# Optimization experiments

Hardware: AMD Instinct MI355X
Metric: run time of the kernel (lower is better)

The kernel has to match this reference:

```python
import jax, jax.numpy as jnp
import numpy as np

ALPHA = 0.2   # LeakyReLU negative slope (init arg alpha)
H = 256       # hidden_dim
U = 1024      # user pairs -> 2U user nodes
M = 64        # UAV nodes
D = 2 * U     # uniform out-degree per UAV (edges sorted by source)
N = 2 * U + M
E = M * D


def _lstm_dir(x, w_ih, w_hh, b):
    # x: [T, B, I] -> outputs [T, B, Hc]; b = b_ih + b_hh (they only ever add)
    Hc = w_hh.shape[1]
    B = x.shape[1]
    def step(carry, xt):
        h, c = carry
        g = xt @ w_ih.T + h @ w_hh.T + b          # [B, 4*Hc], gate order i,f,g,o
        i, f, gg, o = jnp.split(g, 4, axis=-1)
        c = jax.nn.sigmoid(f) * c + jax.nn.sigmoid(i) * jnp.tanh(gg)
        h = jax.nn.sigmoid(o) * jnp.tanh(c)
        return (h, c), h
    h0 = jnp.zeros((B, Hc), x.dtype)
    _, hs = jax.lax.scan(step, (h0, h0), x)
    return hs


def _bilstm(x, wih, whh, b):
    # wih: [2, 4Hc, I]; whh: [2, 4Hc, Hc]; b: [2, 4Hc]; dir 0 = fwd, 1 = reverse
    fwd = _lstm_dir(x, wih[0], whh[0], b[0])
    rev = _lstm_dir(x[::-1], wih[1], whh[1], b[1])[::-1]
    return jnp.concatenate([fwd, rev], axis=-1)   # [T, B, 2*Hc]


def _mlp2(h, w1, b1, w2, b2):
    h = jax.nn.relu(h @ w1.T + b1)
    return jax.nn.relu(h @ w2.T + b2)


def _forward(x, edge_index, users_num,
             ul_wih, ul_whh, ul_b, uav_lin_w, uav_lin_b,
             msg_w1, msg_b1, msg_w2, msg_b2,
             wq_w, wq_b, wr_w, wr_b, att_w, att_b,
             upd_w1, upd_b1, upd_w2, upd_b2,
             uavl_wih, uavl_whh, uavl_b, lin2_w, lin2_b):
    Un = users_num
    n = x.shape[0]
    m = n - 2 * Un
    # ---- users bidirectional LSTM over the pair (seq_len=2, batch=U) ----
    seq = jnp.stack([x[:Un], x[Un:2 * Un]], axis=0)        # [2, U, 2]
    users = _bilstm(seq, ul_wih, ul_whh, ul_b)             # [2, U, H]
    users = jnp.concatenate([users[0], users[1]], axis=0)  # [2U, H]
    uavs = x[2 * Un:] @ uav_lin_w.T + uav_lin_b            # [M, H]
    h = jnp.concatenate([users, uavs], axis=0)             # [N, H]
    # ---- message passing (flow target_to_source: i=src, aggregate at src) ----
    src, tgt = edge_index[0], edge_index[1]
    xi = h[src]                                            # [E, H]
    xj = h[tgt]                                            # [E, H]
    msg = _mlp2(jnp.concatenate([xi, xj], axis=1), msg_w1, msg_b1, msg_w2, msg_b2)  # [E, H]
    q = xi @ wq_w.T + wq_b
    r = msg @ wr_w.T + wr_b
    a = jax.nn.leaky_relu(jnp.concatenate([q, r], axis=1) @ att_w.T + att_b, ALPHA)  # [E,1]
    # segment softmax: edges sorted by source, uniform degree -> reshape [M, D]
    a = jax.nn.softmax(a.reshape(m, -1), axis=1).reshape(-1, 1)
    # ---- scatter-mean aggregate over source index ----
    agg = jax.ops.segment_sum(a * msg, src, num_segments=n)          # [N, H]
    cnt = jax.ops.segment_sum(jnp.ones((src.shape[0],), x.dtype), src, num_segments=n)
    agg = agg / jnp.maximum(cnt, 1.0)[:, None]
    # ---- update ----
    h2 = _mlp2(jnp.concatenate([agg, h], axis=1), upd_w1, upd_b1, upd_w2, upd_b2)  # [N, H]
    uav_seq = h2[2 * Un:][:, None, :]                      # [M, 1, H]
    uav_out = _bilstm(uav_seq, uavl_wih, uavl_whh, uavl_b)[:, 0, :]  # [M, H]
    out = jnp.concatenate([h2[:2 * Un], uav_out], axis=0)
    return jax.nn.sigmoid(out @ lin2_w.T + lin2_b)         # [N, 2]


def setup_inputs():
    key = jax.random.key(0)
    ks = iter(jax.random.split(key, 32))
    p = lambda *s: jax.random.normal(next(ks), s, jnp.float32) * 0.05
    Hc = H // 2
    x = jax.random.uniform(next(ks), (N, 2), jnp.float32)
    src = jnp.repeat(2 * U + jnp.arange(M), D)
    tgt = jnp.tile(jnp.arange(2 * U), M)
    edge_index = jnp.stack([src, tgt]).astype(jnp.int32)
    return dict(
        x=x, edge_index=edge_index, users_num=U,
        ul_wih=p(2, 4 * Hc, 2), ul_whh=p(2, 4 * Hc, Hc), ul_b=p(2, 4 * Hc),
        uav_lin_w=p(H, 2), uav_lin_b=p(H),
        msg_w1=p(H, 2 * H), msg_b1=p(H), msg_w2=p(H, H), msg_b2=p(H),
        wq_w=p(H, H), wq_b=p(H), wr_w=p(H, H), wr_b=p(H),
        att_w=p(1, 2 * H), att_b=p(1),
        upd_w1=p(H, 2 * H), upd_b1=p(H), upd_w2=p(H, H), upd_b2=p(H),
        uavl_wih=p(2, 4 * Hc, H), uavl_whh=p(2, 4 * Hc, Hc), uavl_b=p(2, 4 * Hc),
        lin2_w=p(2, H), lin2_b=p(2),
    )


def reference(x, edge_index, users_num,
              ul_wih, ul_whh, ul_b, uav_lin_w, uav_lin_b,
              msg_w1, msg_b1, msg_w2, msg_b2,
              wq_w, wq_b, wr_w, wr_b, att_w, att_b,
              upd_w1, upd_b1, upd_w2, upd_b2,
              uavl_wih, uavl_whh, uavl_b, lin2_w, lin2_b):
    return _forward(x, edge_index, users_num,
                    ul_wih, ul_whh, ul_b, uav_lin_w, uav_lin_b,
                    msg_w1, msg_b1, msg_w2, msg_b2,
                    wq_w, wq_b, wr_w, wr_b, att_w, att_b,
                    upd_w1, upd_b1, upd_w2, upd_b2,
                    uavl_wih, uavl_whh, uavl_b, lin2_w, lin2_b)
```

## Files before the change

### kernel.cpp

```cpp
#include <hip/hip_runtime.h>
#include <hip/hip_bf16.h>
#include <math.h>

#define UQ   1024
#define NUQ  2048
#define MQ   64
#define NN   2112
#define HD   256

typedef __attribute__((ext_vector_type(4))) float f32x4;
typedef __attribute__((ext_vector_type(8))) __bf16 bf16x8;

#define OFF_HB    0u
#define OFF_HUF   65536u
#define OFF_PUBF  1146880u
#define OFF_PB    2195456u
#define OFF_SPR   2260992u
#define OFF_ATT   2261248u
#define OFF_WHHT  2263552u
#define OFF_WIHT  2787840u
#define OFF_W1F   3836416u
#define OFF_W2F   4098560u
#define OFF_UW1F  4229632u
#define OFF_UW2F  4491776u
#define OFF_CREC  4622848u
#define OFF_H2U   5155328u

__device__ __forceinline__ float sigm(float v) { return 1.f / (1.f + expf(-v)); }

__device__ __forceinline__ int huf_idx(int row, int k) {
  return (((row >> 6) * 8 + (k >> 5)) * 4 + ((row >> 4) & 3)) * 512 +
         (((k >> 3) & 3) * 16 + (row & 15)) * 8 + (k & 7);
}
__device__ __forceinline__ int pubf_idx(int row, int k) {
  return (((row >> 8) * 8 + (k >> 5)) * 16 + ((row >> 4) & 15)) * 512 +
         (((k >> 3) & 3) * 16 + (row & 15)) * 8 + (k & 7);
}

__device__ __forceinline__ void gl16(const void* g, void* l) {
  __builtin_amdgcn_global_load_lds((const __attribute__((address_space(1))) void*)g,
                                   (__attribute__((address_space(3))) void*)l, 16, 0, 0);
}

__device__ void tile_transpose_perm(const float* __restrict__ in, int in_ld,
                                    float* __restrict__ out, int out_ld,
                                    int k0, int c0) {
  __shared__ float ldt[64][68];
  const int t = threadIdx.x;
  {
    const int ci = t >> 2, kq = t & 3;
    const int c = c0 + ci;
    const int row = (c & 3) * 128 + (c >> 2);
    const float* src = in + row * in_ld + k0 + kq * 16;
#pragma unroll
    for (int e = 0; e < 4; ++e)
      *(f32x4*)&ldt[ci][kq * 16 + e * 4] = *(const f32x4*)(src + e * 4);
  }
  __syncthreads();
  {
    const int kk = t >> 2, cq = t & 3;
    float* dst = out + (k0 + kk) * out_ld + c0 + cq * 16;
#pragma unroll
    for (int e4 = 0; e4 < 4; ++e4) {
      f32x4 v;
#pragma unroll
      for (int j = 0; j < 4; ++j) v[j] = ldt[cq * 16 + e4 * 4 + j][kk];
      *(f32x4*)(dst + e4 * 4) = v;
    }
  }
}

template<int K>
__device__ void frag_cast16(const float* __restrict__ W, int j0, __bf16* __restrict__ frag) {
  __shared__ float ldc[16][K + 4];
  const int t = threadIdx.x;
  {
    const int jr = t >> 4, kq = t & 15;
    const float* src = W + (j0 + jr) * K + kq * (K / 16);
#pragma unroll
    for (int e = 0; e < K / 64; ++e)
      *(f32x4*)&ldc[jr][kq * (K / 16) + e * 4] = *(const f32x4*)(src + e * 4);
  }
  __syncthreads();
  const int f = j0 >> 4;
  constexpr int nks = K >> 5;
  constexpr int thr_per_ks = 256 / nks;
  constexpr int q_per_thr = 512 / thr_per_ks;
  const int ks = t / thr_per_ks;
  const int q0 = (t % thr_per_ks) * q_per_thr;
#pragma unroll
  for (int h = 0; h < q_per_thr / 8; ++h) {
    bf16x8 v;
#pragma unroll
    for (int e = 0; e < 8; ++e) {
      int q = q0 + h * 8 + e;
      int lane = q >> 3;
      v[e] = (__bf16)ldc[lane & 15][ks * 32 + (lane >> 4) * 8 + (q & 7)];
    }
    *(bf16x8*)(frag + (ks * 16 + f) * 512 + q0 + h * 8) = v;
  }
}

__global__ __launch_bounds__(256) void k0_prep(
    const float* __restrict__ ul_whh, const float* __restrict__ uavl_wih,
    const float* __restrict__ msg_w1, const float* __restrict__ msg_w2,
    const float* __restrict__ upd_w1, const float* __restrict__ upd_w2,
    const float* __restrict__ att_w,  const float* __restrict__ att_b,
    const float* __restrict__ wq_w,   const float* __restrict__ wq_b,
    const float* __restrict__ wr_w,   const float* __restrict__ wr_b,
    char* __restrict__ ws)
{
  const int b = blockIdx.x, t = threadIdx.x;
  if (b < 32) {
    const int dir = b >> 4, tile = b & 15;
    tile_transpose_perm(ul_whh + dir * 65536, 128,
                        (float*)(ws + OFF_WHHT) + dir * 65536, 512,
                        (tile >> 3) * 64, (tile & 7) * 64);
  } else if (b < 96) {
    const int b2 = b - 32, dir = b2 >> 5, tile = b2 & 31;
    tile_transpose_perm(uavl_wih + dir * 131072, 256,
                        (float*)(ws + OFF_WIHT) + dir * 131072, 512,
                        (tile >> 3) * 64, (tile & 7) * 64);
  } else if (b < 112) {
    frag_cast16<256>(msg_w2, (b - 96) * 16, (__bf16*)(ws + OFF_W2F));
  } else if (b < 128) {
    frag_cast16<512>(msg_w1, (b - 112) * 16, (__bf16*)(ws + OFF_W1F));
  } else if (b < 144) {
    frag_cast16<512>(upd_w1, (b - 128) * 16, (__bf16*)(ws + OFF_UW1F));
  } else if (b < 160) {
    frag_cast16<256>(upd_w2, (b - 144) * 16, (__bf16*)(ws + OFF_UW2F));
  } else {
    float* wqa = (float*)(ws + OFF_ATT);
    float* vv  = wqa + 256;
    float* c0  = wqa + 512;
    float sa = 0.f, sr = 0.f;
    for (int j = 0; j < 256; ++j) {
      sa += att_w[j]       * wq_w[j * 256 + t];
      sr += att_w[256 + j] * wr_w[j * 256 + t];
    }
    wqa[t] = sa; vv[t] = sr;
    __shared__ float red[256];
    red[t] = att_w[t] * wq_b[t] + att_w[256 + t] * wr_b[t];
    __syncthreads();
    for (int s = 128; s > 0; s >>= 1) { if (t < s) red[t] += red[t + s]; __syncthreads(); }
    if (t == 0) c0[0] = red[0] + att_b[0];
  }
}

__global__ __launch_bounds__(256) void k1_embed(
    const float* __restrict__ x, const float* __restrict__ ul_wih,
    const float* __restrict__ ul_b, const float* __restrict__ uav_lin_w,
    const float* __restrict__ uav_lin_b, char* __restrict__ ws)
{
  __bf16* huf = (__bf16*)(ws + OFF_HUF);
  const int b = blockIdx.x, tid = threadIdx.x;
  if (b < 256) {
    const float* whhT = (const float*)(ws + OFF_WHHT);
    const int dir = tid >> 7, hc = tid & 127;
    const int u0 = b * 4;
    float wx[4], wy[4], bb[4];
#pragma unroll
    for (int g = 0; g < 4; ++g) {
      int row = g * 128 + hc;
      wx[g] = ul_wih[dir * 1024 + row * 2 + 0];
      wy[g] = ul_wih[dir * 1024 + row * 2 + 1];
      bb[g] = ul_b[dir * 512 + row];
    }
    __shared__ float h1s[2][128][4];
    __shared__ float hout[8][260];
    float c1[4], h1v[4], in1x[4], in1y[4];
#pragma unroll
    for (int uu = 0; uu < 4; ++uu) {
      int u = u0 + uu;
      float ax = x[u * 2], ay = x[u * 2 + 1];
      float bx = x[(UQ + u) * 2], by = x[(UQ + u) * 2 + 1];
      float i0x = dir ? bx : ax, i0y = dir ? by : ay;
      in1x[uu] = dir ? ax : bx; in1y[uu] = dir ? ay : by;
      float gv[4];
#pragma unroll
      for (int g = 0; g < 4; ++g) gv[g] = wx[g] * i0x + wy[g] * i0y + bb[g];
      float ii = sigm(gv[0]), gg = tanhf(gv[2]), oo = sigm(gv[3]);
      c1[uu] = ii * gg;
      h1v[uu] = oo * tanhf(c1[uu]);
      h1s[dir][hc][uu] = h1v[uu];
    }
    __syncthreads();
    float acc[4][4];
#pragma unroll
    for (int uu = 0; uu < 4; ++uu)
#pragma unroll
      for (int g = 0; g < 4; ++g) acc[uu][g] = wx[g] * in1x[uu] + wy[g] * in1y[uu] + bb[g];
    for (int k = 0; k < 128; ++k) {
      f32x4 hv  = *(const f32x4*)&h1s[dir][k][0];
      f32x4 wv4 = *(const f32x4*)(whhT + dir * 65536 + k * 512 + hc * 4);
#pragma unroll
      for (int uu = 0; uu < 4; ++uu)
#pragma unroll
        for (int g = 0; g < 4; ++g) acc[uu][g] += hv[uu] * wv4[g];
    }
    const int col = dir * 128 + hc;
#pragma unroll
    for (int uu = 0; uu < 4; ++uu) {
      float ii = sigm(acc[uu][0]), ff = sigm(acc[uu][1]);
      float gg = tanhf(acc[uu][2]), oo = sigm(acc[uu][3]);
      float c2 = ff * c1[uu] + ii * gg;
      float h2v = oo * tanhf(c2);
      float va = dir ? h2v : h1v[uu];
      float vb = dir ? h1v[uu] : h2v;
      hout[uu][col] = va;
      hout[4 + uu][col] = vb;
    }
    __syncthreads();
    {
      const int lr = tid >> 5, c = tid & 31;
      bf16x8 v;
#pragma unroll
      for (int e = 0; e < 8; ++e) v[e] = (__bf16)hout[lr][c * 8 + e];
      const int node = (lr < 4) ? (u0 + lr) : (UQ + u0 + lr - 4);
      *(bf16x8*)(huf + huf_idx(node, c * 8)) = v;
    }
  } else {
    float* hb = (float*)(ws + OFF_HB);
    const int j = tid;
    const int mb = (b - 256) * 16;
    for (int m = mb; m < mb + 16; ++m) {
      float xa = x[(NUQ + m) * 2], xb = x[(NUQ + m) * 2 + 1];
      float val = xa * uav_lin_w[j * 2] + xb * uav_lin_w[j * 2 + 1] + uav_lin_b[j];
      hb[m * 256 + j] = val;
      huf[huf_idx(NUQ + m, j)] = (__bf16)val;
    }
  }
}

template<int NKS>
__device__ __forceinline__ void frag_gemm_acc(const __bf16* __restrict__ Abase,
                                              const __bf16* __restrict__ Bbase,
                                              f32x4 acc[4][4]) {
  const int lane = threadIdx.x & 63;
  const int cg = threadIdx.x >> 6;
  for (int ks = 0; ks < NKS; ++ks) {
    bf16x8 Af[4], Bf[4];
#pragma unroll
    for (int g = 0; g < 4; ++g)
      Af[g] = *(const bf16x8*)(Abase + ((ks * 4 + g) * 64 + lane) * 8);
#pragma unroll
    for (int f = 0; f < 4; ++f)
      Bf[f] = *(const bf16x8*)(Bbase + ((ks * 16 + cg * 4 + f) * 64 + lane) * 8);
#pragma unroll
    for (int g = 0; g < 4; ++g)
#pragma unroll
      for (int f = 0; f < 4; ++f)
        acc[g][f] = __builtin_amdgcn_mfma_f32_16x16x32_bf16(Af[g], Bf[f], acc[g][f], 0, 0, 0);
  }
}

__global__ __launch_bounds__(256) void k2_proj(const float* __restrict__ msg_b1,
                                               char* __restrict__ ws)
{
  const __bf16* huf = (const __bf16*)(ws + OFF_HUF);
  const __bf16* w1f = (const __bf16*)(ws + OFF_W1F);
  const int b = blockIdx.x;
  const int lane = threadIdx.x & 63, cg = threadIdx.x >> 6;
  const int cl = lane & 15, g16 = lane >> 4;
  if (b < 32) {
    f32x4 acc[4][4] = {};
    frag_gemm_acc<8>(huf + b * 16384, w1f + 65536, acc);
    __bf16* pubf = (__bf16*)(ws + OFF_PUBF);
#pragma unroll
    for (int g = 0; g < 4; ++g)
#pragma unroll
      for (int f = 0; f < 4; ++f)
#pragma unroll
        for (int r = 0; r < 4; ++r) {
          int row = b * 64 + g * 16 + g16 * 4 + r;
          int col = cg * 64 + f * 16 + cl;
          pubf[pubf_idx(row, col)] = (__bf16)acc[g][f][r];
        }
  } else if (b == 32) {
    f32x4 acc[4][4] = {};
    frag_gemm_acc<8>(huf + 32 * 16384, w1f, acc);
    float* pb = (float*)(ws + OFF_PB);
#pragma unroll
    for (int g = 0; g < 4; ++g)
#pragma unroll
      for (int f = 0; f < 4; ++f)
#pragma unroll
        for (int r = 0; r < 4; ++r) {
          int row = g * 16 + g16 * 4 + r;
          int col = cg * 64 + f * 16 + cl;
          pb[row * 256 + col] = acc[g][f][r] + msg_b1[col];
        }
  } else {
    const float* hb  = (const float*)(ws + OFF_HB);
    const float* wqa = (const float*)(ws + OFF_ATT);
    const float* c0  = wqa + 512;
    float* spr = (float*)(ws + OFF_SPR);
    const int t = threadIdx.x;
    if (t < 64) {
      float s = 0.f;
      for (int k = 0; k < 256; ++k) s += hb[t * 256 + k] * wqa[k];
      spr[t] = s + c0[0];
    }
  }
}

__global__ __launch_bounds__(1024, 2) void k3_edge(const float* __restrict__ msg_b2,
                                                   char* __restrict__ ws)
{
  const char*  PUBF = (const char*)(ws + OFF_PUBF);
  const float* PB   = (const float*)(ws + OFF_PB);
  const float* spr  = (const float*)(ws + OFF_SPR);
  const float* vv   = (const float*)(ws + OFF_ATT) + 256;
  const char*  W2F  = (const char*)(ws + OFF_W2F);
  float* crec = (float*)(ws + OFF_CREC);

  __shared__ __align__(16) char bufA[2][16384];
  __shared__ __align__(16) char bufB[2][16384];
  __shared__ float plds[16][64];
  __shared__ float redmax[16], wds[16];
  __shared__ float wvs[4][256];

  const int m = blockIdx.x >> 3, ch = blockIdx.x & 7;
  const int tid = threadIdx.x, wave = tid >> 6, lane = tid & 63;
  const int cl = lane & 15, g16 = lane >> 4;
  const int rg = wave >> 2, cg = wave & 3;
  const float sm = spr[m];
  const char* Asrc = PUBF + ch * 131072;
  const float* pbm = PB + m * 256;

  {
    bf16x8 araw = *(const bf16x8*)(Asrc + wave * 1024 + lane * 16);
    gl16(W2F + wave * 1024 + lane * 16, &bufB[0][wave * 1024]);
    const float* pbp = pbm + (lane >> 4) * 8;
    f32x4 p0 = *(const f32x4*)pbp, p1 = *(const f32x4*)(pbp + 4);
    bf16x8 a;
#pragma unroll
    for (int r = 0; r < 4; ++r) {
      a[r]     = (__bf16)fmaxf((float)araw[r]     + p0[r], 0.f);
      a[4 + r] = (__bf16)fmaxf((float)araw[4 + r] + p1[r], 0.f);
    }
    *(bf16x8*)(&bufA[0][wave * 1024 + lane * 16]) = a;
  }
  __syncthreads();

  f32x4 acc[4][4] = {};
  for (int ks = 0; ks < 8; ++ks) {
    const int cur = ks & 1;
    bf16x8 arn{};
    f32x4 pn0{}, pn1{};
    if (ks < 7) {
      arn = *(const bf16x8*)(Asrc + (ks + 1) * 16384 + wave * 1024 + lane * 16);
      gl16(W2F + (ks + 1) * 16384 + wave * 1024 + lane * 16, &bufB[cur ^ 1][wave * 1024]);
      const float* pbp = pbm + (ks + 1) * 32 + (lane >> 4) * 8;
      pn0 = *(const f32x4*)pbp;
      pn1 = *(const f32x4*)(pbp + 4);
    }
    bf16x8 Af[4], Bf[4];
#pragma unroll
    for (int g = 0; g < 4; ++g)
      Af[g] = *(const bf16x8*)(&bufA[cur][((rg * 4 + g) * 64 + lane) * 16]);
#pragma unroll
    for (int f = 0; f < 4; ++f)
      Bf[f] = *(const bf16x8*)(&bufB[cur][((cg * 4 + f) * 64 + lane) * 16]);
#pragma unroll
    for (int g = 0; g < 4; ++g)
#pragma unroll
      for (int f = 0; f < 4; ++f)
        acc[g][f] = __builtin_amdgcn_mfma_f32_16x16x32_bf16(Af[g], Bf[f], acc[g][f], 0, 0, 0);
    if (ks < 7) {
      bf16x8 a;
#pragma unroll
      for (int r = 0; r < 4; ++r) {
        a[r]     = (__bf16)fmaxf((float)arn[r]     + pn0[r], 0.f);
        a[4 + r] = (__bf16)fmaxf((float)arn[4 + r] + pn1[r], 0.f);
      }
      *(bf16x8*)(&bufA[cur ^ 1][wave * 1024 + lane * 16]) = a;
    }
    __syncthreads();
  }

  float p[4][4] = {};
#pragma unroll
  for (int f = 0; f < 4; ++f) {
    const int j = cg * 64 + f * 16 + cl;
    const float b2j = msg_b2[j], vj = vv[j];
#pragma unroll
    for (int g = 0; g < 4; ++g)
#pragma unroll
      for (int r = 0; r < 4; ++r) {
        float mv = fmaxf(acc[g][f][r] + b2j, 0.f);
        acc[g][f][r] = mv;
        p[g][r] += mv * vj;
      }
  }
#pragma unroll
  for (int mask = 1; mask < 16; mask <<= 1)
#pragma unroll
    for (int g = 0; g < 4; ++g)
#pragma unroll
      for (int r = 0; r < 4; ++r) p[g][r] += __shfl_xor(p[g][r], mask);
  if (cl == 0) {
#pragma unroll
    for (int g = 0; g < 4; ++g)
#pragma unroll
      for (int r = 0; r < 4; ++r) plds[wave][g * 16 + g16 * 4 + r] = p[g][r];
  }
  __syncthreads();

  float lr[4][4], wm = -3.4e38f;
#pragma unroll
  for (int g = 0; g < 4; ++g)
#pragma unroll
    for (int r = 0; r < 4; ++r) {
      int row = g * 16 + g16 * 4 + r;
      float l = plds[rg * 4 + 0][row] + plds[rg * 4 + 1][row] +
                plds[rg * 4 + 2][row] + plds[rg * 4 + 3][row] + sm;
      l = l > 0.f ? l : 0.2f * l;
      lr[g][r] = l;
      wm = fmaxf(wm, l);
    }
  wm = fmaxf(wm, __shfl_xor(wm, 16));
  wm = fmaxf(wm, __shfl_xor(wm, 32));
  if (lane == 0) redmax[wave] = wm;
  __syncthreads();
  float Mc = redmax[0];
#pragma unroll
  for (int i = 1; i < 16; ++i) Mc = fmaxf(Mc, redmax[i]);

  float e[4][4], ds = 0.f;
#pragma unroll
  for (int g = 0; g < 4; ++g)
#pragma unroll
    for (int r = 0; r < 4; ++r) { e[g][r] = __expf(lr[g][r] - Mc); ds += e[g][r]; }
  ds += __shfl_xor(ds, 16);
  ds += __shfl_xor(ds, 32);
  if (lane == 0) wds[wave] = ds;

#pragma unroll
  for (int f = 0; f < 4; ++f) {
    float w = 0.f;
#pragma unroll
    for (int g = 0; g < 4; ++g)
#pragma unroll
      for (int r = 0; r < 4; ++r) w += e[g][r] * acc[g][f][r];
    w += __shfl_xor(w, 16);
    w += __shfl_xor(w, 32);
    if (g16 == 0) wvs[rg][cg * 64 + f * 16 + cl] = w;
  }
  __syncthreads();

  float* rec = crec + (m * 8 + ch) * 260;
  if (tid < 256) rec[tid] = wvs[0][tid] + wvs[1][tid] + wvs[2][tid] + wvs[3][tid];
  if (tid == 0) rec[256] = Mc;
  if (tid == 1) rec[257] = wds[0] + wds[4] + wds[8] + wds[12];
}

__global__ __launch_bounds__(256) void k56_update(
    const float* __restrict__ upd_b1, const float* __restrict__ upd_b2,
    const float* __restrict__ lin2_w, const float* __restrict__ lin2_b,
    float* __restrict__ out, char* __restrict__ ws)
{
  const __bf16* huf  = (const __bf16*)(ws + OFF_HUF);
  const __bf16* uw1f = (const __bf16*)(ws + OFF_UW1F);
  const __bf16* uw2f = (const __bf16*)(ws + OFF_UW2F);

  __shared__ __align__(16) __bf16 l1f[8 * 4 * 512];
  __shared__ __align__(16) __bf16 aggf[8 * 4 * 512];
  __shared__ float scs[64][8];
  __shared__ float sS[64];
  __shared__ float l2p[4][64][2];

  const int b = blockIdx.x, tid = threadIdx.x;
  const int lane = tid & 63, cg = tid >> 6;
  const int cl = lane & 15, g16 = lane >> 4;

  f32x4 acc[4][4] = {};
  if (b < 32) {
    frag_gemm_acc<8>(huf + b * 16384, uw1f + 8 * 16 * 512, acc);
  } else {
    const float* crec = (const float*)(ws + OFF_CREC);
    if (tid < 64) {
      const int m = tid;
      float mx = -3.4e38f;
      for (int c = 0; c < 8; ++c) mx = fmaxf(mx, crec[(m * 8 + c) * 260 + 256]);
      float S = 0.f;
      for (int c = 0; c < 8; ++c) {
        float sc = __expf(crec[(m * 8 + c) * 260 + 256] - mx);
        scs[m][c] = sc;
        S += sc * crec[(m * 8 + c) * 260 + 257];
      }
      sS[m] = S;
    }
    __syncthreads();
    for (int m = 0; m < 64; ++m) {
      float A = 0.f;
#pragma unroll
      for (int c = 0; c < 8; ++c) A += scs[m][c] * crec[(m * 8 + c) * 260 + tid];
      float agg = A / sS[m] * (1.f / 2048.f);
      aggf[((tid >> 5) * 4 + (m >> 4)) * 512 + (((tid >> 3) & 3) * 16 + (m & 15)) * 8 + (tid & 7)] =
          (__bf16)agg;
    }
    __syncthreads();
    const __bf16* hufu = huf + 32 * 16384;
    for (int ks = 0; ks < 8; ++ks) {
      bf16x8 Af[4], Bf[4];
#pragma unroll
      for (int g = 0; g < 4; ++g)
        Af[g] = *(const bf16x8*)(aggf + ((ks * 4 + g) * 64 + lane) * 8);
#pragma unroll
      for (int f = 0; f < 4; ++f)
        Bf[f] = *(const bf16x8*)(uw1f + ((ks * 16 + cg * 4 + f) * 64 + lane) * 8);
#pragma unroll
      for (int g = 0; g < 4; ++g)
#pragma unroll
        for (int f = 0; f < 4; ++f)
          acc[g][f] = __builtin_amdgcn_mfma_f32_16x16x32_bf16(Af[g], Bf[f], acc[g][f], 0, 0, 0);
    }
    for (int ks = 8; ks < 16; ++ks) {
      bf16x8 Af[4], Bf[4];
#pragma unroll
      for (int g = 0; g < 4; ++g)
        Af[g] = *(const bf16x8*)(hufu + (((ks - 8) * 4 + g) * 64 + lane) * 8);
#pragma unroll
      for (int f = 0; f < 4; ++f)
        Bf[f] = *(const bf16x8*)(uw1f + ((ks * 16 + cg * 4 + f) * 64 + lane) * 8);
#pragma unroll
      for (int g = 0; g < 4; ++g)
#pragma unroll
        for (int f = 0; f < 4; ++f)
          acc[g][f] = __builtin_amdgcn_mfma_f32_16x16x32_bf16(Af[g], Bf[f], acc[g][f], 0, 0, 0);
    }
  }

#pragma unroll
  for (int g = 0; g < 4; ++g)
#pragma unroll
    for (int f = 0; f < 4; ++f) {
      const int col = cg * 64 + f * 16 + cl;
      const float b1 = upd_b1[col];
#pragma unroll
      for (int r = 0; r < 4; ++r) {
        const int rl = g * 16 + g16 * 4 + r;
        float v = fmaxf(acc[g][f][r] + b1, 0.f);
        l1f[((col >> 5) * 4 + g) * 512 + (((col >> 3) & 3) * 16 + (rl & 15)) * 8 + (col & 7)] =
            (__bf16)v;
      }
    }
  __syncthreads();

  f32x4 a2[4][4] = {};
  for (int ks = 0; ks < 8; ++ks) {
    bf16x8 Af[4], Bf[4];
#pragma unroll
    for (int g = 0; g < 4; ++g)
      Af[g] = *(const bf16x8*)(l1f + ((ks * 4 + g) * 64 + lane) * 8);
#pragma unroll
    for (int f = 0; f < 4; ++f)
      Bf[f] = *(const bf16x8*)(uw2f + ((ks * 16 + cg * 4 + f) * 64 + lane) * 8);
#pragma unroll
    for (int g = 0; g < 4; ++g)
#pragma unroll
      for (int f = 0; f < 4; ++f)
        a2[g][f] = __builtin_amdgcn_mfma_f32_16x16x32_bf16(Af[g], Bf[f], a2[g][f], 0, 0, 0);
  }

  if (b < 32) {
    float d0[4][4] = {}, d1[4][4] = {};
#pragma unroll
    for (int f = 0; f < 4; ++f) {
      const int col = cg * 64 + f * 16 + cl;
      const float b2 = upd_b2[col];
      const float w0 = lin2_w[col], w1 = lin2_w[256 + col];
#pragma unroll
      for (int g = 0; g < 4; ++g)
#pragma unroll
        for (int r = 0; r < 4; ++r) {
          float hv = fmaxf(a2[g][f][r] + b2, 0.f);
          d0[g][r] += hv * w0;
          d1[g][r] += hv * w1;
        }
    }
#pragma unroll
    for (int mask = 1; mask < 16; mask <<= 1)
#pragma unroll
      for (int g = 0; g < 4; ++g)
#pragma unroll
        for (int r = 0; r < 4; ++r) {
          d0[g][r] += __shfl_xor(d0[g][r], mask);
          d1[g][r] += __shfl_xor(d1[g][r], mask);
        }
    if (cl == 0) {
#pragma unroll
      for (int g = 0; g < 4; ++g)
#pragma unroll
        for (int r = 0; r < 4; ++r) {
          l2p[cg][g * 16 + g16 * 4 + r][0] = d0[g][r];
          l2p[cg][g * 16 + g16 * 4 + r][1] = d1[g][r];
        }
    }
    __syncthreads();
    if (tid < 64) {
      float s0 = l2p[0][tid][0] + l2p[1][tid][0] + l2p[2][tid][0] + l2p[3][tid][0] + lin2_b[0];
      float s1 = l2p[0][tid][1] + l2p[1][tid][1] + l2p[2][tid][1] + l2p[3][tid][1] + lin2_b[1];
      const int row = b * 64 + tid;
      out[row * 2 + 0] = 1.f / (1.f + expf(-s0));
      out[row * 2 + 1] = 1.f / (1.f + expf(-s1));
    }
  } else {
    float* h2u = (float*)(ws + OFF_H2U);
#pragma unroll
    for (int g = 0; g < 4; ++g)
#pragma unroll
      for (int f = 0; f < 4; ++f) {
        const int col = cg * 64 + f * 16 + cl;
        const float b2 = upd_b2[col];
#pragma unroll
        for (int r = 0; r < 4; ++r) {
          const int rl = g * 16 + g16 * 4 + r;
          h2u[rl * 256 + col] = fmaxf(a2[g][f][r] + b2, 0.f);
        }
      }
  }
}

__global__ __launch_bounds__(256) void k7_final(
    const float* __restrict__ uavl_b, const float* __restrict__ lin2_w,
    const float* __restrict__ lin2_b, float* __restrict__ out, char* __restrict__ ws)
{
  const float* h2u = (const float*)(ws + OFF_H2U);
  const int b = blockIdx.x, tid = threadIdx.x;
  const float* wihT = (const float*)(ws + OFF_WIHT);
  __shared__ float xs[256], uo[256];
  xs[tid] = h2u[b * 256 + tid];
  __syncthreads();
  const int dir = tid >> 7, hc = tid & 127;
  float a4[4] = {0.f, 0.f, 0.f, 0.f};
  for (int k = 0; k < 256; ++k) {
    float xv = xs[k];
    f32x4 wv4 = *(const f32x4*)(wihT + dir * 131072 + k * 512 + hc * 4);
#pragma unroll
    for (int g = 0; g < 4; ++g) a4[g] += xv * wv4[g];
  }
  float bb[4];
#pragma unroll
  for (int g = 0; g < 4; ++g) bb[g] = uavl_b[dir * 512 + g * 128 + hc];
  float ii = sigm(a4[0] + bb[0]);
  float gg = tanhf(a4[2] + bb[2]);
  float oo = sigm(a4[3] + bb[3]);
  float cc = ii * gg;
  uo[dir * 128 + hc] = oo * tanhf(cc);
  __syncthreads();
  float p0 = uo[tid] * lin2_w[tid];
  float p1 = uo[tid] * lin2_w[256 + tid];
#pragma unroll
  for (int mask = 1; mask < 64; mask <<= 1) {
    p0 += __shfl_xor(p0, mask);
    p1 += __shfl_xor(p1, mask);
  }
  __shared__ float r0s[4], r1s[4];
  const int lane = tid & 63, wv = tid >> 6;
  if (lane == 0) { r0s[wv] = p0; r1s[wv] = p1; }
  __syncthreads();
  if (tid == 0) {
    float d0 = r0s[0] + r0s[1] + r0s[2] + r0s[3] + lin2_b[0];
    float d1 = r1s[0] + r1s[1] + r1s[2] + r1s[3] + lin2_b[1];
    out[(NUQ + b) * 2 + 0] = 1.f / (1.f + expf(-d0));
    out[(NUQ + b) * 2 + 1] = 1.f / (1.f + expf(-d1));
  }
}

extern "C" void kernel_launch(void* const* d_in, const int* in_sizes, int n_in,
                              void* d_out, int out_size, void* d_ws, size_t ws_size,
                              hipStream_t stream)
{
  const float* x         = (const float*)d_in[0];
  const float* ul_wih    = (const float*)d_in[3];
  const float* ul_whh    = (const float*)d_in[4];
  const float* ul_b      = (const float*)d_in[5];
  const float* uav_lin_w = (const float*)d_in[6];
  const float* uav_lin_b = (const float*)d_in[7];
  const float* msg_w1    = (const float*)d_in[8];
  const float* msg_b1    = (const float*)d_in[9];
  const float* msg_w2    = (const float*)d_in[10];
  const float* msg_b2    = (const float*)d_in[11];
  const float* wq_w      = (const float*)d_in[12];
  const float* wq_b      = (const float*)d_in[13];
  const float* wr_w      = (const float*)d_in[14];
  const float* wr_b      = (const float*)d_in[15];
  const float* att_w     = (const float*)d_in[16];
  const float* att_b     = (const float*)d_in[17];
  const float* upd_w1    = (const float*)d_in[18];
  const float* upd_b1    = (const float*)d_in[19];
  const float* upd_w2    = (const float*)d_in[20];
  const float* upd_b2    = (const float*)d_in[21];
  const float* uavl_wih  = (const float*)d_in[22];
  const float* uavl_b    = (const float*)d_in[24];
  const float* lin2_w    = (const float*)d_in[25];
  const float* lin2_b    = (const float*)d_in[26];
  char* ws = (char*)d_ws;
  float* out = (float*)d_out;

  k0_prep<<<dim3(161), dim3(256), 0, stream>>>(ul_whh, uavl_wih, msg_w1, msg_w2, upd_w1,
                                               upd_w2, att_w, att_b, wq_w, wq_b, wr_w, wr_b, ws);
  k1_embed<<<dim3(260), dim3(256), 0, stream>>>(x, ul_wih, ul_b, uav_lin_w, uav_lin_b, ws);
  k2_proj<<<dim3(34), dim3(256), 0, stream>>>(msg_b1, ws);
  k3_edge<<<dim3(512), dim3(1024), 0, stream>>>(msg_b2, ws);
  k56_update<<<dim3(33), dim3(256), 0, stream>>>(upd_b1, upd_b2, lin2_w, lin2_b, out, ws);
  k7_final<<<dim3(64), dim3(256), 0, stream>>>(uavl_b, lin2_w, lin2_b, out, ws);
}
```

Baseline: 110.8 us.

## Split GEMM kernels into finer row blocks and split final gate GEMV over K

After: 94.51 us. 14.7% less time.

```diff
diff --git a/kernel.cpp b/kernel.cpp
--- a/kernel.cpp
+++ b/kernel.cpp
@@ -25,6 +25,7 @@
 #define OFF_UW2F  4491776u
 #define OFF_CREC  4622848u
 #define OFF_H2U   5155328u
+#define OFF_PART  5220864u
 
 __device__ __forceinline__ float sigm(float v) { return 1.f / (1.f + expf(-v)); }
 
@@ -232,22 +233,22 @@
   }
 }
 
-template<int NKS>
-__device__ __forceinline__ void frag_gemm_acc(const __bf16* __restrict__ Abase,
-                                              const __bf16* __restrict__ Bbase,
-                                              f32x4 acc[4][4]) {
+template<int G, int NKS>
+__device__ __forceinline__ void frag_gemm_acc_g(const __bf16* __restrict__ Abase, int g0,
+                                                const __bf16* __restrict__ Bbase,
+                                                f32x4 acc[G][4]) {
   const int lane = threadIdx.x & 63;
   const int cg = threadIdx.x >> 6;
   for (int ks = 0; ks < NKS; ++ks) {
-    bf16x8 Af[4], Bf[4];
-#pragma unroll
-    for (int g = 0; g < 4; ++g)
-      Af[g] = *(const bf16x8*)(Abase + ((ks * 4 + g) * 64 + lane) * 8);
+    bf16x8 Af[G], Bf[4];
+#pragma unroll
+    for (int g = 0; g < G; ++g)
+      Af[g] = *(const bf16x8*)(Abase + ((ks * 4 + g0 + g) * 64 + lane) * 8);
 #pragma unroll
     for (int f = 0; f < 4; ++f)
       Bf[f] = *(const bf16x8*)(Bbase + ((ks * 16 + cg * 4 + f) * 64 + lane) * 8);
 #pragma unroll
-    for (int g = 0; g < 4; ++g)
+    for (int g = 0; g < G; ++g)
 #pragma unroll
       for (int f = 0; f < 4; ++f)
         acc[g][f] = __builtin_amdgcn_mfma_f32_16x16x32_bf16(Af[g], Bf[f], acc[g][f], 0, 0, 0);
@@ -262,23 +263,23 @@
   const int b = blockIdx.x;
   const int lane = threadIdx.x & 63, cg = threadIdx.x >> 6;
   const int cl = lane & 15, g16 = lane >> 4;
-  if (b < 32) {
-    f32x4 acc[4][4] = {};
-    frag_gemm_acc<8>(huf + b * 16384, w1f + 65536, acc);
+  if (b < 64) {
+    f32x4 acc[2][4] = {};
+    frag_gemm_acc_g<2, 8>(huf + (b >> 1) * 16384, (b & 1) * 2, w1f + 65536, acc);
     __bf16* pubf = (__bf16*)(ws + OFF_PUBF);
 #pragma unroll
-    for (int g = 0; g < 4; ++g)
+    for (int g = 0; g < 2; ++g)
 #pragma unroll
       for (int f = 0; f < 4; ++f)
 #pragma unroll
         for (int r = 0; r < 4; ++r) {
-          int row = b * 64 + g * 16 + g16 * 4 + r;
+          int row = b * 32 + g * 16 + g16 * 4 + r;
           int col = cg * 64 + f * 16 + cl;
           pubf[pubf_idx(row, col)] = (__bf16)acc[g][f][r];
         }
-  } else if (b == 32) {
+  } else if (b == 64) {
     f32x4 acc[4][4] = {};
-    frag_gemm_acc<8>(huf + 32 * 16384, w1f, acc);
+    frag_gemm_acc_g<4, 8>(huf + 32 * 16384, 0, w1f, acc);
     float* pb = (float*)(ws + OFF_PB);
 #pragma unroll
     for (int g = 0; g < 4; ++g)
@@ -324,14 +325,15 @@
   const int tid = threadIdx.x, wave = tid >> 6, lane = tid & 63;
   const int cl = lane & 15, g16 = lane >> 4;
   const int rg = wave >> 2, cg = wave & 3;
+  const int rot = (m + ch) & 7;
   const float sm = spr[m];
   const char* Asrc = PUBF + ch * 131072;
   const float* pbm = PB + m * 256;
 
   {
-    bf16x8 araw = *(const bf16x8*)(Asrc + wave * 1024 + lane * 16);
-    gl16(W2F + wave * 1024 + lane * 16, &bufB[0][wave * 1024]);
-    const float* pbp = pbm + (lane >> 4) * 8;
+    bf16x8 araw = *(const bf16x8*)(Asrc + rot * 16384 + wave * 1024 + lane * 16);
+    gl16(W2F + rot * 16384 + wave * 1024 + lane * 16, &bufB[0][wave * 1024]);
+    const float* pbp = pbm + rot * 32 + (lane >> 4) * 8;
     f32x4 p0 = *(const f32x4*)pbp, p1 = *(const f32x4*)(pbp + 4);
     bf16x8 a;
 #pragma unroll
@@ -344,14 +346,15 @@
   __syncthreads();
 
   f32x4 acc[4][4] = {};
-  for (int ks = 0; ks < 8; ++ks) {
-    const int cur = ks & 1;
+  for (int i = 0; i < 8; ++i) {
+    const int cur = i & 1;
     bf16x8 arn{};
     f32x4 pn0{}, pn1{};
-    if (ks < 7) {
-      arn = *(const bf16x8*)(Asrc + (ks + 1) * 16384 + wave * 1024 + lane * 16);
-      gl16(W2F + (ks + 1) * 16384 + wave * 1024 + lane * 16, &bufB[cur ^ 1][wave * 1024]);
-      const float* pbp = pbm + (ks + 1) * 32 + (lane >> 4) * 8;
+    if (i < 7) {
+      const int ksn = (i + 1 + rot) & 7;
+      arn = *(const bf16x8*)(Asrc + ksn * 16384 + wave * 1024 + lane * 16);
+      gl16(W2F + ksn * 16384 + wave * 1024 + lane * 16, &bufB[cur ^ 1][wave * 1024]);
+      const float* pbp = pbm + ksn * 32 + (lane >> 4) * 8;
       pn0 = *(const f32x4*)pbp;
       pn1 = *(const f32x4*)(pbp + 4);
     }
@@ -362,12 +365,14 @@
 #pragma unroll
     for (int f = 0; f < 4; ++f)
       Bf[f] = *(const bf16x8*)(&bufB[cur][((cg * 4 + f) * 64 + lane) * 16]);
+    __builtin_amdgcn_s_setprio(1);
 #pragma unroll
     for (int g = 0; g < 4; ++g)
 #pragma unroll
       for (int f = 0; f < 4; ++f)
         acc[g][f] = __builtin_amdgcn_mfma_f32_16x16x32_bf16(Af[g], Bf[f], acc[g][f], 0, 0, 0);
-    if (ks < 7) {
+    __builtin_amdgcn_s_setprio(0);
+    if (i < 7) {
       bf16x8 a;
 #pragma unroll
       for (int r = 0; r < 4; ++r) {
@@ -464,68 +469,70 @@
   const __bf16* uw1f = (const __bf16*)(ws + OFF_UW1F);
   const __bf16* uw2f = (const __bf16*)(ws + OFF_UW2F);
 
-  __shared__ __align__(16) __bf16 l1f[8 * 4 * 512];
-  __shared__ __align__(16) __bf16 aggf[8 * 4 * 512];
-  __shared__ float scs[64][8];
-  __shared__ float sS[64];
-  __shared__ float l2p[4][64][2];
+  __shared__ __align__(16) __bf16 l1f[8 * 2 * 512];
+  __shared__ __align__(16) __bf16 aggf[8 * 2 * 512];
+  __shared__ float scs[32][8];
+  __shared__ float sS[32];
+  __shared__ float l2p[4][32][2];
 
   const int b = blockIdx.x, tid = threadIdx.x;
   const int lane = tid & 63, cg = tid >> 6;
   const int cl = lane & 15, g16 = lane >> 4;
 
-  f32x4 acc[4][4] = {};
-  if (b < 32) {
-    frag_gemm_acc<8>(huf + b * 16384, uw1f + 8 * 16 * 512, acc);
+  f32x4 acc[2][4] = {};
+  if (b < 64) {
+    frag_gemm_acc_g<2, 8>(huf + (b >> 1) * 16384, (b & 1) * 2, uw1f + 8 * 16 * 512, acc);
   } else {
+    const int m0 = (b - 64) * 32;
     const float* crec = (const float*)(ws + OFF_CREC);
-    if (tid < 64) {
-      const int m = tid;
+    if (tid < 32) {
+      const int m = m0 + tid;
       float mx = -3.4e38f;
       for (int c = 0; c < 8; ++c) mx = fmaxf(mx, crec[(m * 8 + c) * 260 + 256]);
       float S = 0.f;
       for (int c = 0; c < 8; ++c) {
         float sc = __expf(crec[(m * 8 + c) * 260 + 256] - mx);
-        scs[m][c] = sc;
+        scs[tid][c] = sc;
         S += sc * crec[(m * 8 + c) * 260 + 257];
       }
-      sS[m] = S;
+      sS[tid] = S;
     }
     __syncthreads();
-    for (int m = 0; m < 64; ++m) {
+    for (int ml = 0; ml < 32; ++ml) {
       float A = 0.f;
 #pragma unroll
-      for (int c = 0; c < 8; ++c) A += scs[m][c] * crec[(m * 8 + c) * 260 + tid];
-      float agg = A / sS[m] * (1.f / 2048.f);
-      aggf[((tid >> 5) * 4 + (m >> 4)) * 512 + (((tid >> 3) & 3) * 16 + (m & 15)) * 8 + (tid & 7)] =
+      for (int c = 0; c < 8; ++c) A += scs[ml][c] * crec[((m0 + ml) * 8 + c) * 260 + tid];
+      float agg = A / sS[ml] * (1.f / 2048.f);
+      aggf[((tid >> 5) * 2 + (ml >> 4)) * 512 + (((tid >> 3) & 3) * 16 + (ml & 15)) * 8 + (tid & 7)] =
           (__bf16)agg;
     }
     __syncthreads();
+    const int g0 = (b - 64) * 2;
     const __bf16* hufu = huf + 32 * 16384;
     for (int ks = 0; ks < 8; ++ks) {
-      bf16x8 Af[4], Bf[4];
-#pragma unroll
-      for (int g = 0; g < 4; ++g)
-        Af[g] = *(const bf16x8*)(aggf + ((ks * 4 + g) * 64 + lane) * 8);
+      bf16x8 Af[2], Bf[4];
+#pragma unroll
+      for (int g = 0; g < 2; ++g)
+        Af[g] = *(const bf16x8*)(aggf + ((ks * 2 + g) * 64 + lane) * 8);
 #pragma unroll
       for (int f = 0; f < 4; ++f)
         Bf[f] = *(const bf16x8*)(uw1f + ((ks * 16 + cg * 4 + f) * 64 + lane) * 8);
 #pragma unroll
-      for (int g = 0; g < 4; ++g)
+      for (int g = 0; g < 2; ++g)
 #pragma unroll
         for (int f = 0; f < 4; ++f)
           acc[g][f] = __builtin_amdgcn_mfma_f32_16x16x32_bf16(Af[g], Bf[f], acc[g][f], 0, 0, 0);
     }
     for (int ks = 8; ks < 16; ++ks) {
-      bf16x8 Af[4], Bf[4];
-#pragma unroll
-      for (int g = 0; g < 4; ++g)
-        Af[g] = *(const bf16x8*)(hufu + (((ks - 8) * 4 + g) * 64 + lane) * 8);
+      bf16x8 Af[2], Bf[4];
+#pragma unroll
+      for (int g = 0; g < 2; ++g)
+        Af[g] = *(const bf16x8*)(hufu + (((ks - 8) * 4 + g0 + g) * 64 + lane) * 8);
 #pragma unroll
       for (int f = 0; f < 4; ++f)
         Bf[f] = *(const bf16x8*)(uw1f + ((ks * 16 + cg * 4 + f) * 64 + lane) * 8);
 #pragma unroll
-      for (int g = 0; g < 4; ++g)
+      for (int g = 0; g < 2; ++g)
 #pragma unroll
         for (int f = 0; f < 4; ++f)
           acc[g][f] = __builtin_amdgcn_mfma_f32_16x16x32_bf16(Af[g], Bf[f], acc[g][f], 0, 0, 0);
@@ -533,46 +540,45 @@
   }
 
 #pragma unroll
-  for (int g = 0; g < 4; ++g)
+  for (int g = 0; g < 2; ++g)
 #pragma unroll
     for (int f = 0; f < 4; ++f) {
       const int col = cg * 64 + f * 16 + cl;
       const float b1 = upd_b1[col];
 #pragma unroll
       for (int r = 0; r < 4; ++r) {
-        const int rl = g * 16 + g16 * 4 + r;
         float v = fmaxf(acc[g][f][r] + b1, 0.f);
-        l1f[((col >> 5) * 4 + g) * 512 + (((col >> 3) & 3) * 16 + (rl & 15)) * 8 + (col & 7)] =
+        l1f[((col >> 5) * 2 + g) * 512 + (((col >> 3) & 3) * 16 + g16 * 4 + r) * 8 + (col & 7)] =
             (__bf16)v;
       }
     }
   __syncthreads();
 
-  f32x4 a2[4][4] = {};
+  f32x4 a2[2][4] = {};
   for (int ks = 0; ks < 8; ++ks) {
-    bf16x8 Af[4], Bf[4];
-#pragma unroll
-    for (int g = 0; g < 4; ++g)
-      Af[g] = *(const bf16x8*)(l1f + ((ks * 4 + g) * 64 + lane) * 8);
+    bf16x8 Af[2], Bf[4];
+#pragma unroll
+    for (int g = 0; g < 2; ++g)
+      Af[g] = *(const bf16x8*)(l1f + ((ks * 2 + g) * 64 + lane) * 8);
 #pragma unroll
     for (int f = 0; f < 4; ++f)
       Bf[f] = *(const bf16x8*)(uw2f + ((ks * 16 + cg * 4 + f) * 64 + lane) * 8);
 #pragma unroll
-    for (int g = 0; g < 4; ++g)
+    for (int g = 0; g < 2; ++g)
 #pragma unroll
       for (int f = 0; f < 4; ++f)
         a2[g][f] = __builtin_amdgcn_mfma_f32_16x16x32_bf16(Af[g], Bf[f], a2[g][f], 0, 0, 0);
   }
 
-  if (b < 32) {
-    float d0[4][4] = {}, d1[4][4] = {};
+  if (b < 64) {
+    float d0[2][4] = {}, d1[2][4] = {};
 #pragma unroll
     for (int f = 0; f < 4; ++f) {
       const int col = cg * 64 + f * 16 + cl;
       const float b2 = upd_b2[col];
       const float w0 = lin2_w[col], w1 = lin2_w[256 + col];
 #pragma unroll
-      for (int g = 0; g < 4; ++g)
+      for (int g = 0; g < 2; ++g)
 #pragma unroll
         for (int r = 0; r < 4; ++r) {
           float hv = fmaxf(a2[g][f][r] + b2, 0.f);
@@ -583,7 +589,7 @@
 #pragma unroll
     for (int mask = 1; mask < 16; mask <<= 1)
 #pragma unroll
-      for (int g = 0; g < 4; ++g)
+      for (int g = 0; g < 2; ++g)
 #pragma unroll
         for (int r = 0; r < 4; ++r) {
           d0[g][r] += __shfl_xor(d0[g][r], mask);
@@ -591,7 +597,7 @@
         }
     if (cl == 0) {
 #pragma unroll
-      for (int g = 0; g < 4; ++g)
+      for (int g = 0; g < 2; ++g)
 #pragma unroll
         for (int r = 0; r < 4; ++r) {
           l2p[cg][g * 16 + g16 * 4 + r][0] = d0[g][r];
@@ -599,17 +605,18 @@
         }
     }
     __syncthreads();
-    if (tid < 64) {
+    if (tid < 32) {
       float s0 = l2p[0][tid][0] + l2p[1][tid][0] + l2p[2][tid][0] + l2p[3][tid][0] + lin2_b[0];
       float s1 = l2p[0][tid][1] + l2p[1][tid][1] + l2p[2][tid][1] + l2p[3][tid][1] + lin2_b[1];
-      const int row = b * 64 + tid;
+      const int row = b * 32 + tid;
       out[row * 2 + 0] = 1.f / (1.f + expf(-s0));
       out[row * 2 + 1] = 1.f / (1.f + expf(-s1));
     }
   } else {
     float* h2u = (float*)(ws + OFF_H2U);
-#pragma unroll
-    for (int g = 0; g < 4; ++g)
+    const int m0 = (b - 64) * 32;
+#pragma unroll
+    for (int g = 0; g < 2; ++g)
 #pragma unroll
       for (int f = 0; f < 4; ++f) {
         const int col = cg * 64 + f * 16 + cl;
@@ -617,33 +624,51 @@
 #pragma unroll
         for (int r = 0; r < 4; ++r) {
           const int rl = g * 16 + g16 * 4 + r;
-          h2u[rl * 256 + col] = fmaxf(a2[g][f][r] + b2, 0.f);
+          h2u[(m0 + rl) * 256 + col] = fmaxf(a2[g][f][r] + b2, 0.f);
         }
       }
   }
 }
 
-__global__ __launch_bounds__(256) void k7_final(
+__global__ __launch_bounds__(256) void k7a_gates(char* __restrict__ ws)
+{
+  const float* h2u  = (const float*)(ws + OFF_H2U);
+  const float* wihT = (const float*)(ws + OFF_WIHT);
+  float* part = (float*)(ws + OFF_PART);
+  const int m = blockIdx.x >> 2, kq = blockIdx.x & 3;
+  const int tid = threadIdx.x;
+  const int dir = tid >> 7, hc = tid & 127;
+  __shared__ float xs[64];
+  if (tid < 64) xs[tid] = h2u[m * 256 + kq * 64 + tid];
+  __syncthreads();
+  f32x4 a4 = {0.f, 0.f, 0.f, 0.f};
+  for (int k = 0; k < 64; ++k) {
+    float xv = xs[k];
+    f32x4 wv4 = *(const f32x4*)(wihT + dir * 131072 + (kq * 64 + k) * 512 + hc * 4);
+#pragma unroll
+    for (int g = 0; g < 4; ++g) a4[g] += xv * wv4[g];
+  }
+  *(f32x4*)(part + (m * 4 + kq) * 1024 + dir * 512 + hc * 4) = a4;
+}
+
+__global__ __launch_bounds__(256) void k7b_final(
     const float* __restrict__ uavl_b, const float* __restrict__ lin2_w,
     const float* __restrict__ lin2_b, float* __restrict__ out, char* __restrict__ ws)
 {
-  const float* h2u = (const float*)(ws + OFF_H2U);
-  const int b = blockIdx.x, tid = threadIdx.x;
-  const float* wihT = (const float*)(ws + OFF_WIHT);
-  __shared__ float xs[256], uo[256];
-  xs[tid] = h2u[b * 256 + tid];
-  __syncthreads();
+  const float* part = (const float*)(ws + OFF_PART);
+  const int m = blockIdx.x, tid = threadIdx.x;
   const int dir = tid >> 7, hc = tid & 127;
-  float a4[4] = {0.f, 0.f, 0.f, 0.f};
-  for (int k = 0; k < 256; ++k) {
-    float xv = xs[k];
-    f32x4 wv4 = *(const f32x4*)(wihT + dir * 131072 + k * 512 + hc * 4);
-#pragma unroll
-    for (int g = 0; g < 4; ++g) a4[g] += xv * wv4[g];
+  f32x4 a4 = {0.f, 0.f, 0.f, 0.f};
+#pragma unroll
+  for (int kq = 0; kq < 4; ++kq) {
+    f32x4 p = *(const f32x4*)(part + (m * 4 + kq) * 1024 + dir * 512 + hc * 4);
+#pragma unroll
+    for (int g = 0; g < 4; ++g) a4[g] += p[g];
   }
   float bb[4];
 #pragma unroll
   for (int g = 0; g < 4; ++g) bb[g] = uavl_b[dir * 512 + g * 128 + hc];
+  __shared__ float uo[256];
   float ii = sigm(a4[0] + bb[0]);
   float gg = tanhf(a4[2] + bb[2]);
   float oo = sigm(a4[3] + bb[3]);
@@ -664,8 +689,8 @@
   if (tid == 0) {
     float d0 = r0s[0] + r0s[1] + r0s[2] + r0s[3] + lin2_b[0];
     float d1 = r1s[0] + r1s[1] + r1s[2] + r1s[3] + lin2_b[1];
-    out[(NUQ + b) * 2 + 0] = 1.f / (1.f + expf(-d0));
-    out[(NUQ + b) * 2 + 1] = 1.f / (1.f + expf(-d1));
+    out[(NUQ + m) * 2 + 0] = 1.f / (1.f + expf(-d0));
+    out[(NUQ + m) * 2 + 1] = 1.f / (1.f + expf(-d1));
   }
 }
 
@@ -703,8 +728,9 @@
   k0_prep<<<dim3(161), dim3(256), 0, stream>>>(ul_whh, uavl_wih, msg_w1, msg_w2, upd_w1,
                                                upd_w2, att_w, att_b, wq_w, wq_b, wr_w, wr_b, ws);
   k1_embed<<<dim3(260), dim3(256), 0, stream>>>(x, ul_wih, ul_b, uav_lin_w, uav_lin_b, ws);
-  k2_proj<<<dim3(34), dim3(256), 0, stream>>>(msg_b1, ws);
+  k2_proj<<<dim3(66), dim3(256), 0, stream>>>(msg_b1, ws);
   k3_edge<<<dim3(512), dim3(1024), 0, stream>>>(msg_b2, ws);
-  k56_update<<<dim3(33), dim3(256), 0, stream>>>(upd_b1, upd_b2, lin2_w, lin2_b, out, ws);
-  k7_final<<<dim3(64), dim3(256), 0, stream>>>(uavl_b, lin2_w, lin2_b, out, ws);
-}
+  k56_update<<<dim3(66), dim3(256), 0, stream>>>(upd_b1, upd_b2, lin2_w, lin2_b, out, ws);
+  k7a_gates<<<dim3(256), dim3(256), 0, stream>>>(ws);
+  k7b_final<<<dim3(64), dim3(256), 0, stream>>>(uavl_b, lin2_w, lin2_b, out, ws);
+}
```
